# Kernel tuning notes

Measured on AMD Instinct MI355X. Metric: run time of the kernel, lower is better.

Reference implementation:

```python
import jax, jax.numpy as jnp
import numpy as np

EPS = 1e-5  # torch InstanceNorm2d default eps


def _attend(x_q, x_kv, Wq, Wk, Wv, Wo):
    # x_q, x_kv: [B, N, C]
    B, N, _ = x_q.shape
    q = x_q @ Wq            # [B, N, CH]
    k = x_kv @ Wk           # [B, N, CH]
    v = x_kv @ Wv           # [B, N, CH]
    CH = q.shape[-1]
    # rearrange 'b n c -> n (b c)' : [N, B*CH]; the torch repeat across batch
    # is redundant (same K/V for every query sample), so we keep one copy.
    kcat = jnp.transpose(k, (1, 0, 2)).reshape(N, B * CH)
    vcat = jnp.transpose(v, (1, 0, 2)).reshape(N, B * CH)
    # scores[b, i, j] = sum_n q[b, n, i] * kcat[n, j]  -> [B, CH, B*CH]
    scores = jnp.einsum('bni,nj->bij', q, kcat)
    # InstanceNorm2d(1): per-sample normalization over the (CH, B*CH) plane
    mu = scores.mean(axis=(1, 2), keepdims=True)
    var = scores.var(axis=(1, 2), keepdims=True)  # biased var, matches torch
    scores = (scores - mu) * jax.lax.rsqrt(var + EPS)
    attn = jax.nn.softmax(scores, axis=-1)        # softmax over j (dim=3)
    # ctx[b, n, i] = sum_j attn[b, i, j] * vcat[n, j]  -> [B, N, CH]
    ctx = jnp.einsum('bij,nj->bni', attn, vcat)
    return ctx @ Wo  # [B, N, C]


def setup_inputs() -> dict:
    key = jax.random.key(0)
    k0, k1, k2, k3, k4 = jax.random.split(key, 5)
    C, H = 64, 8
    CH = C * H
    emb = jax.random.normal(k0, (16, 2048, C), dtype=jnp.float32)
    s = 0.02
    Wq = jax.random.normal(k1, (C, CH), dtype=jnp.float32) * s
    Wk = jax.random.normal(k2, (C, CH), dtype=jnp.float32) * s
    Wv = jax.random.normal(k3, (C, CH), dtype=jnp.float32) * s
    Wo = jax.random.normal(k4, (CH, C), dtype=jnp.float32) * s
    return {"emb": emb, "Wq": Wq, "Wk": Wk, "Wv": Wv, "Wo": Wo}


def reference(emb, Wq, Wk, Wv, Wo):
    emb_l, emb_u = jnp.split(emb, 2, axis=0)
    emb_u_sg = jax.lax.stop_gradient(emb_u)  # emb_u is detached in the torch code
    out_u2l = _attend(emb_u_sg, emb_l, Wq, Wk, Wv, Wo)
    out_l2u = _attend(emb_l, emb_u_sg, Wq, Wk, Wv, Wo)
    return jnp.concatenate([out_l2u, out_u2l], axis=0)
```

## Files before the change

### kernel.cpp

```cpp
#include <hip/hip_runtime.h>
#include <hip/hip_fp16.h>

#define EPS 1e-5f

typedef __attribute__((ext_vector_type(8))) _Float16 half8;
typedef __attribute__((ext_vector_type(4))) _Float16 half4;
typedef __attribute__((ext_vector_type(4))) float float4v;

__device__ __forceinline__ float rv_from(const float* sums2, int db)
{
    float s1 = 0.f, s2 = 0.f;
#pragma unroll
    for (int p = 0; p < 8; p++) {
        s1 += sums2[(db * 8 + p) * 2];
        s2 += sums2[(db * 8 + p) * 2 + 1];
    }
    const float inv = 1.f / 2097152.f;
    float mu = s1 * inv;
    float var = s2 * inv - mu * mu;
    return rsqrtf(var + EPS);
}

__global__ __launch_bounds__(256)
void convT_k(const float* __restrict__ emb, const float* __restrict__ Wq,
             const float* __restrict__ Wk, const float* __restrict__ Wv,
             const float* __restrict__ Wo, __half* __restrict__ emb16,
             __half* __restrict__ embT16, __half* __restrict__ WkT16,
             __half* __restrict__ Wo16, __half* __restrict__ Wv16,
             float* __restrict__ GWQpart, float* __restrict__ wsp,
             __half* __restrict__ WqT16h, __half* __restrict__ WqT16l)
{
    __shared__ __align__(16) char smem[18432];
    const int tid = threadIdx.x;
    const int bid = blockIdx.x;

    if (bid < 256) {
        __half (*T)[136] = (__half(*)[136])smem;
        const int bb = bid >> 4;
        const int t0 = (bid & 15) * 128;
        const float* src = emb + (long long)bb * 131072 + (long long)t0 * 64;
        __half* d16 = emb16 + (long long)bb * 131072 + (long long)t0 * 64;
#pragma unroll
        for (int it = 0; it < 8; it++) {
            int e = (tid + it * 256) * 4;
            int t = e >> 6, c = e & 63;
            float4 v = *(const float4*)(src + t * 64 + c);
            half4 h;
            h[0] = (_Float16)v.x; h[1] = (_Float16)v.y;
            h[2] = (_Float16)v.z; h[3] = (_Float16)v.w;
            *(half4*)(d16 + t * 64 + c) = h;
            T[c + 0][t] = (__half)h[0];
            T[c + 1][t] = (__half)h[1];
            T[c + 2][t] = (__half)h[2];
            T[c + 3][t] = (__half)h[3];
        }
        __syncthreads();
        __half* dT = embT16 + (long long)bb * 131072 + t0;
#pragma unroll
        for (int it = 0; it < 4; it++) {
            int e = (tid + it * 256) * 8;
            int c = e >> 7, tt = e & 127;
            *(half8*)(dT + (long long)c * 2048 + tt) = *(const half8*)&T[c][tt];
        }
    } else if (bid < 272) {
        float (*t)[65] = (float(*)[65])smem;
        const int which = (bid - 256) >> 3;
        const int c0 = ((bid - 256) & 7) * 64;
        const int c = tid & 63, r4 = tid >> 6;
        if (which == 0) {
#pragma unroll
            for (int rr = r4; rr < 64; rr += 4)
                t[rr][c] = Wk[rr * 512 + c0 + c];
            __syncthreads();
#pragma unroll
            for (int rr = r4; rr < 64; rr += 4)
                WkT16[(c0 + rr) * 64 + c] = __float2half(t[c][rr]);
        } else {
#pragma unroll
            for (int rr = r4; rr < 64; rr += 4)
                t[rr][c] = Wo[(c0 + rr) * 64 + c];
            __syncthreads();
#pragma unroll
            for (int rr = r4; rr < 64; rr += 4)
                Wo16[rr * 512 + c0 + c] = __float2half(t[c][rr]);
        }
    } else if (bid < 280) {
        const int base = (bid - 272) * 4096;
#pragma unroll
        for (int it = 0; it < 4; it++) {
            int e = base + (tid + it * 256) * 4;
            float4 v = *(const float4*)(Wv + e);
            *(__half2*)(Wv16 + e)     = __floats2half2_rn(v.x, v.y);
            *(__half2*)(Wv16 + e + 2) = __floats2half2_rn(v.z, v.w);
        }
    } else if (bid < 296) {
        float (*Wl)[68] = (float(*)[68])smem;
        const int t2 = bid - 280;
        const int which = t2 >> 3;
        const int sl = t2 & 7;
        const int i0 = sl * 64;
        const float* W = which ? Wq : Wk;
        float* Gout = GWQpart + (long long)(which * 8 + sl) * 4096;
#pragma unroll
        for (int it = 0; it < 4; it++) {
            int e = tid + it * 256;
            int cc = e >> 4, i4 = (e & 15) * 4;
            *(float4*)&Wl[cc][i4] = *(const float4*)(W + cc * 512 + i0 + i4);
        }
        __syncthreads();
        if (tid < 64) {
            float s = 0.f;
#pragma unroll
            for (int j = 0; j < 64; j++) s += Wl[tid][j];
            wsp[(which * 8 + sl) * 64 + tid] = s;
        }
        const int cr = tid >> 2, cg = (tid & 3) * 16;
        float p[16] = {};
        for (int k = 0; k < 64; k++) {
            float a = Wl[cr][k];
#pragma unroll
            for (int j = 0; j < 16; j++) p[j] += a * Wl[cg + j][k];
        }
#pragma unroll
        for (int j = 0; j < 16; j++)
            Gout[cr * 64 + cg + j] = p[j];
    } else {
        float (*t)[65] = (float(*)[65])smem;
        const int i0 = (bid - 296) * 64;
        const int c = tid & 63, r4 = tid >> 6;
#pragma unroll
        for (int rr = r4; rr < 64; rr += 4)
            t[rr][c] = Wq[rr * 512 + i0 + c];
        __syncthreads();
#pragma unroll
        for (int rr = r4; rr < 64; rr += 4) {
            float x = t[c][rr];
            __half h = __float2half(x);
            WqT16h[(i0 + rr) * 64 + c] = h;
            WqT16l[(i0 + rr) * 64 + c] = __float2half(x - __half2float(h));
        }
    }
}

__global__ __launch_bounds__(256)
void gram_k(const __half* __restrict__ embT16, float* __restrict__ Gpart)
{
    const int tid = threadIdx.x, bid = blockIdx.x;
    const int ks = bid >> 6, z6 = bid & 63;
    const int b = z6 >> 3, bp = z6 & 7;
    const int lane = tid & 63, w = tid >> 6, q = lane >> 4, l16 = lane & 15;

    const __half* Arow = embT16 + (long long)b * 131072 +
                         (long long)(w * 16 + l16) * 2048 + ks * 256 + q * 8;
    const __half* Bbase = embT16 + 1048576 + (long long)bp * 131072 +
                          (long long)l16 * 2048 + ks * 256 + q * 8;

    float4v acc[4];
#pragma unroll
    for (int nt = 0; nt < 4; nt++) acc[nt] = (float4v)0.f;

#pragma unroll
    for (int t0 = 0; t0 < 256; t0 += 32) {
        half8 af = *(const half8*)(Arow + t0);
        half8 bf[4];
#pragma unroll
        for (int nt = 0; nt < 4; nt++)
            bf[nt] = *(const half8*)(Bbase + nt * 32768 + t0);
#pragma unroll
        for (int nt = 0; nt < 4; nt++)
            acc[nt] = __builtin_amdgcn_mfma_f32_16x16x32_f16(af, bf[nt], acc[nt], 0, 0, 0);
    }

    float* Gz = Gpart + (long long)ks * 262144 + (long long)z6 * 4096;
#pragma unroll
    for (int nt = 0; nt < 4; nt++)
#pragma unroll
        for (int t = 0; t < 4; t++) {
            int m = w * 16 + q * 4 + t;
            Gz[m * 64 + nt * 16 + l16] = acc[nt][t];
        }
}

__global__ __launch_bounds__(256)
void stats2_k(const float* __restrict__ Gpart, const float* __restrict__ GWQpart,
              const float* __restrict__ wsp, __half* __restrict__ GT16h,
              __half* __restrict__ GT16l, float* __restrict__ sums2)
{
    __shared__ float Graw[64][68], Gs[64][68], GQs[64][68], GWs[64][68];
    __shared__ float wqsS[64], wksS[64];
    const int tid = threadIdx.x;
    const int z = blockIdx.x;
    const int d = z >> 6, b = (z >> 3) & 7, bp = z & 7;
    const int zm = d ? (bp * 8 + b) : (b * 8 + bp);

    for (int f = tid * 4; f < 4096; f += 1024) {
        float4 g = make_float4(0.f, 0.f, 0.f, 0.f);
        float4 gw = g, gq = g;
#pragma unroll
        for (int s = 0; s < 8; s++) {
            float4 p = *(const float4*)(Gpart + (long long)s * 262144 + (long long)zm * 4096 + f);
            g.x += p.x; g.y += p.y; g.z += p.z; g.w += p.w;
            float4 w1 = *(const float4*)(GWQpart + (long long)s * 4096 + f);
            gw.x += w1.x; gw.y += w1.y; gw.z += w1.z; gw.w += w1.w;
            float4 q1 = *(const float4*)(GWQpart + (long long)(8 + s) * 4096 + f);
            gq.x += q1.x; gq.y += q1.y; gq.z += q1.z; gq.w += q1.w;
        }
        int rr = f >> 6, cc = f & 63;
        *(float4*)&Graw[rr][cc] = g;
        *(float4*)&GWs[rr][cc] = gw;
        *(float4*)&GQs[rr][cc] = gq;
    }
    if (tid < 64) {
        float a = 0.f, bsum = 0.f;
#pragma unroll
        for (int s = 0; s < 8; s++) {
            bsum += wsp[s * 64 + tid];
            a    += wsp[(8 + s) * 64 + tid];
        }
        wqsS[tid] = a; wksS[tid] = bsum;
    }
    __syncthreads();
    for (int e = tid; e < 4096; e += 256) {
        int rr = e >> 6, cc = e & 63;
        Gs[rr][cc] = d ? Graw[cc][rr] : Graw[rr][cc];
    }
    __syncthreads();
    for (int e = tid; e < 4096; e += 256) {
        int cp = e >> 6, c = e & 63;
        float g = Gs[c][cp];
        __half h = __float2half(g);
        GT16h[(long long)z * 4096 + e] = h;
        GT16l[(long long)z * 4096 + e] = __float2half(g - __half2float(h));
    }

    const int r = tid >> 2;
    const int c0 = (tid & 3) * 16;
    float p1[16] = {}, p2[16] = {};
    for (int k = 0; k < 64; k++) {
        float gq = GQs[r][k], g = Gs[r][k];
#pragma unroll
        for (int j = 0; j < 16; j++) {
            p1[j] += gq * Gs[k][c0 + j];
            p2[j] += g  * GWs[k][c0 + j];
        }
    }
    float s2 = 0.f;
#pragma unroll
    for (int j = 0; j < 16; j++) s2 += p1[j] * p2[j];
    float s1 = 0.f;
    const float wq = wqsS[r];
#pragma unroll
    for (int j = 0; j < 16; j++) s1 += wq * Gs[r][c0 + j] * wksS[c0 + j];

    const int lane = tid & 63, w = tid >> 6;
#pragma unroll
    for (int off = 32; off; off >>= 1) {
        s1 += __shfl_down(s1, off, 64);
        s2 += __shfl_down(s2, off, 64);
    }
    __shared__ float r1[4], r2[4];
    if (lane == 0) { r1[w] = s1; r2[w] = s2; }
    __syncthreads();
    if (tid == 0) {
        sums2[z * 2]     = r1[0] + r1[1] + r1[2] + r1[3];
        sums2[z * 2 + 1] = r2[0] + r2[1] + r2[2] + r2[3];
    }
}

__global__ __launch_bounds__(256)
void mfma_ms(const __half* __restrict__ WqT16h, const __half* __restrict__ WqT16l,
             const __half* __restrict__ GT16h, const __half* __restrict__ GT16l,
             const __half* __restrict__ WkT16, const __half* __restrict__ Wv16,
             const float* __restrict__ sums2, float* __restrict__ rsp,
             __half* __restrict__ Mt)
{
    __shared__ __half Es[128][72];
    __shared__ __half Wks[2][64][72];
    __shared__ __half Wvs[2][64][72];
    __shared__ __half Pt[128][72];

    const int tid = threadIdx.x;
    const int z = blockIdx.x;
    const int it = blockIdx.y;
    const int db = z >> 3, bp = z & 7;
    const int i0base = it * 128;

    const int lane = tid & 63, w = tid >> 6, q = lane >> 4, l16 = lane & 15;
    const float rv = rv_from(sums2, db);
    const int srow = tid >> 2, sc8 = (tid & 3) * 16;

    half8 gk0 = *(const half8*)(WkT16 + (long long)srow * 64 + sc8);
    half8 gk1 = *(const half8*)(WkT16 + (long long)srow * 64 + sc8 + 8);
    half8 gv0 = *(const half8*)(Wv16 + (long long)srow * 512 + sc8);
    half8 gv1 = *(const half8*)(Wv16 + (long long)srow * 512 + sc8 + 8);

    {
        const __half* Wh = WqT16h + (long long)i0base * 64;
        const __half* Wl = WqT16l + (long long)i0base * 64;
        const __half* Gh = GT16h + (long long)z * 4096;
        const __half* Gl = GT16l + (long long)z * 4096;
        float4v eacc[2][4];
#pragma unroll
        for (int a = 0; a < 2; a++)
#pragma unroll
            for (int b2 = 0; b2 < 4; b2++) eacc[a][b2] = (float4v)0.f;
#pragma unroll
        for (int kc = 0; kc < 64; kc += 32) {
            half8 ah[2], al[2], bh[4], bl[4];
#pragma unroll
            for (int mt = 0; mt < 2; mt++) {
                const int i = w * 32 + mt * 16 + l16;
                ah[mt] = *(const half8*)(Wh + i * 64 + kc + q * 8);
                al[mt] = *(const half8*)(Wl + i * 64 + kc + q * 8);
            }
#pragma unroll
            for (int nt = 0; nt < 4; nt++) {
                const int cp = nt * 16 + l16;
                bh[nt] = *(const half8*)(Gh + cp * 64 + kc + q * 8);
                bl[nt] = *(const half8*)(Gl + cp * 64 + kc + q * 8);
            }
#pragma unroll
            for (int mt = 0; mt < 2; mt++)
#pragma unroll
                for (int nt = 0; nt < 4; nt++) {
                    eacc[mt][nt] = __builtin_amdgcn_mfma_f32_16x16x32_f16(ah[mt], bh[nt], eacc[mt][nt], 0, 0, 0);
                    eacc[mt][nt] = __builtin_amdgcn_mfma_f32_16x16x32_f16(ah[mt], bl[nt], eacc[mt][nt], 0, 0, 0);
                    eacc[mt][nt] = __builtin_amdgcn_mfma_f32_16x16x32_f16(al[mt], bh[nt], eacc[mt][nt], 0, 0, 0);
                }
        }
#pragma unroll
        for (int mt = 0; mt < 2; mt++)
#pragma unroll
            for (int nt = 0; nt < 4; nt++)
#pragma unroll
                for (int t = 0; t < 4; t++)
                    Es[w * 32 + mt * 16 + q * 4 + t][nt * 16 + l16] =
                        __float2half(eacc[mt][nt][t]);
    }
    *(half8*)&Wks[0][srow][sc8]     = gk0;
    *(half8*)&Wks[0][srow][sc8 + 8] = gk1;
    *(half8*)&Wvs[0][srow][sc8]     = gv0;
    *(half8*)&Wvs[0][srow][sc8 + 8] = gv1;
    __syncthreads();

    float4v macc[2][4];
#pragma unroll
    for (int a = 0; a < 2; a++)
#pragma unroll
        for (int b2 = 0; b2 < 4; b2++) macc[a][b2] = (float4v)0.f;
    float rsacc[2] = {0.f, 0.f};

    int cur = 0;
    for (int c = 0; c < 8; c++) {
        const int ch0 = c * 64;
        if (c < 7) {
            const int chn = ch0 + 64;
            gk0 = *(const half8*)(WkT16 + (long long)(chn + srow) * 64 + sc8);
            gk1 = *(const half8*)(WkT16 + (long long)(chn + srow) * 64 + sc8 + 8);
            gv0 = *(const half8*)(Wv16 + (long long)srow * 512 + chn + sc8);
            gv1 = *(const half8*)(Wv16 + (long long)srow * 512 + chn + sc8 + 8);
        }

        float4v sacc[4][2];
#pragma unroll
        for (int a = 0; a < 4; a++)
#pragma unroll
            for (int b2 = 0; b2 < 2; b2++) sacc[a][b2] = (float4v)0.f;
#pragma unroll
        for (int kc = 0; kc < 64; kc += 32) {
            half8 af[4], bf[2];
#pragma unroll
            for (int mt = 0; mt < 4; mt++)
                af[mt] = *(const half8*)&Wks[cur][mt * 16 + l16][kc + q * 8];
#pragma unroll
            for (int nt = 0; nt < 2; nt++)
                bf[nt] = *(const half8*)&Es[w * 32 + nt * 16 + l16][kc + q * 8];
#pragma unroll
            for (int mt = 0; mt < 4; mt++)
#pragma unroll
                for (int nt = 0; nt < 2; nt++)
                    sacc[mt][nt] = __builtin_amdgcn_mfma_f32_16x16x32_f16(af[mt], bf[nt], sacc[mt][nt], 0, 0, 0);
        }

#pragma unroll
        for (int nt = 0; nt < 2; nt++) {
            const int i = w * 32 + nt * 16 + l16;
#pragma unroll
            for (int mt = 0; mt < 4; mt++) {
                float e0 = __expf(rv * sacc[mt][nt][0]);
                float e1 = __expf(rv * sacc[mt][nt][1]);
                float e2 = __expf(rv * sacc[mt][nt][2]);
                float e3 = __expf(rv * sacc[mt][nt][3]);
                rsacc[nt] += e0 + e1 + e2 + e3;
                const int ch = mt * 16 + q * 4;
                *(__half2*)&Pt[i][ch]     = __floats2half2_rn(e0, e1);
                *(__half2*)&Pt[i][ch + 2] = __floats2half2_rn(e2, e3);
            }
        }

#pragma unroll
        for (int kc = 0; kc < 64; kc += 32) {
            half8 af2[2], bf2[4];
#pragma unroll
            for (int mt2 = 0; mt2 < 2; mt2++)
                af2[mt2] = *(const half8*)&Pt[w * 32 + mt2 * 16 + l16][kc + q * 8];
#pragma unroll
            for (int nt2 = 0; nt2 < 4; nt2++)
                bf2[nt2] = *(const half8*)&Wvs[cur][nt2 * 16 + l16][kc + q * 8];
#pragma unroll
            for (int mt2 = 0; mt2 < 2; mt2++)
#pragma unroll
                for (int nt2 = 0; nt2 < 4; nt2++)
                    macc[mt2][nt2] = __builtin_amdgcn_mfma_f32_16x16x32_f16(af2[mt2], bf2[nt2], macc[mt2][nt2], 0, 0, 0);
        }

        if (c < 7) {
            *(half8*)&Wks[cur ^ 1][srow][sc8]     = gk0;
            *(half8*)&Wks[cur ^ 1][srow][sc8 + 8] = gk1;
            *(half8*)&Wvs[cur ^ 1][srow][sc8]     = gv0;
            *(half8*)&Wvs[cur ^ 1][srow][sc8 + 8] = gv1;
        }
        __syncthreads();
        cur ^= 1;
    }

#pragma unroll
    for (int nt = 0; nt < 2; nt++) {
        float p = rsacc[nt];
        p += __shfl_xor(p, 16, 64);
        p += __shfl_xor(p, 32, 64);
        if (q == 0)
            rsp[(long long)(db * 512 + i0base + w * 32 + nt * 16 + l16) * 8 + bp] = p;
    }

    __half (*MtS)[144] = (__half(*)[144])&Pt[0][0];
    const float sc = 1.f / 4096.f;
#pragma unroll
    for (int mt2 = 0; mt2 < 2; mt2++)
#pragma unroll
        for (int nt2 = 0; nt2 < 4; nt2++) {
            const int cp = nt2 * 16 + l16;
            const int il = w * 32 + mt2 * 16 + q * 4;
#pragma unroll
            for (int t = 0; t < 4; t++)
                MtS[cp][il + t] = __float2half(macc[mt2][nt2][t] * sc);
        }
    __syncthreads();
    __half* Mz = Mt + (long long)z * 32768;
    {
        const int row = tid >> 2, seg = (tid & 3) * 32;
#pragma unroll
        for (int j = 0; j < 4; j++)
            *(half8*)(Mz + (long long)row * 512 + i0base + seg + j * 8) =
                *(const half8*)&MtS[row][seg + j * 8];
    }
}

__global__ __launch_bounds__(256)
void mfma_n(const __half* __restrict__ Mt, const __half* __restrict__ Wo16,
            const float* __restrict__ rsp, __half* __restrict__ NT)
{
    __shared__ __half Mts[64][72];
    __shared__ __half Wos[64][72];
    __shared__ float invrS[64];
    const int tid = threadIdx.x;
    const int db = blockIdx.x >> 3, bp = blockIdx.x & 7;
    const __half* Mz = Mt + (long long)(db * 8 + bp) * 32768;
    const int lane = tid & 63, w = tid >> 6, q = lane >> 4, l16 = lane & 15;

    float4v acc[4];
#pragma unroll
    for (int mt = 0; mt < 4; mt++) acc[mt] = (float4v)0.f;

    const int srow = tid >> 2, sc8 = (tid & 3) * 16;

    for (int i0 = 0; i0 < 512; i0 += 64) {
        __syncthreads();
        if (tid < 64) {
            const float* rp = rsp + (long long)(db * 512 + i0 + tid) * 8;
            float4 a = *(const float4*)rp;
            float4 b = *(const float4*)(rp + 4);
            invrS[tid] = 4096.0f / (a.x + a.y + a.z + a.w + b.x + b.y + b.z + b.w);
        }
        __syncthreads();
#pragma unroll
        for (int h = 0; h < 2; h++) {
            half8 v = *(const half8*)(Mz + (long long)srow * 512 + i0 + sc8 + h * 8);
            half8 o;
#pragma unroll
            for (int j = 0; j < 8; j++)
                o[j] = (_Float16)((float)v[j] * invrS[sc8 + h * 8 + j]);
            *(half8*)&Mts[srow][sc8 + h * 8] = o;
            *(half8*)&Wos[srow][sc8 + h * 8] =
                *(const half8*)(Wo16 + (long long)srow * 512 + i0 + sc8 + h * 8);
        }
        __syncthreads();
#pragma unroll
        for (int kc = 0; kc < 64; kc += 32) {
            half8 af[4];
#pragma unroll
            for (int mt = 0; mt < 4; mt++)
                af[mt] = *(const half8*)&Mts[mt * 16 + l16][kc + q * 8];
            half8 bf = *(const half8*)&Wos[w * 16 + l16][kc + q * 8];
#pragma unroll
            for (int mt = 0; mt < 4; mt++)
                acc[mt] = __builtin_amdgcn_mfma_f32_16x16x32_f16(af[mt], bf, acc[mt], 0, 0, 0);
        }
    }

    __half* Nz = NT + (long long)db * 32768;
    const int o = w * 16 + l16;
#pragma unroll
    for (int mt = 0; mt < 4; mt++) {
        const int k = bp * 64 + mt * 16 + q * 4;
        *(__half2*)(Nz + (long long)o * 512 + k)     = __floats2half2_rn(acc[mt][0], acc[mt][1]);
        *(__half2*)(Nz + (long long)o * 512 + k + 2) = __floats2half2_rn(acc[mt][2], acc[mt][3]);
    }
}

__global__ __launch_bounds__(256)
void mfma_out(const __half* __restrict__ emb16, const __half* __restrict__ NT,
              float* __restrict__ out)
{
    const int tid = threadIdx.x;
    const int db = blockIdx.y;
    const int d = db >> 3;
    const int n0 = blockIdx.x * 128;
    const __half* Xb = emb16 + (long long)(1 - d) * 1048576;
    const __half* Bz = NT + (long long)db * 32768;

    const int lane = tid & 63, w = tid >> 6, q = lane >> 4, l16 = lane & 15;

    float4v acc[2][4];
#pragma unroll
    for (int a = 0; a < 2; a++)
#pragma unroll
        for (int b = 0; b < 4; b++) acc[a][b] = (float4v)0.f;

    for (int bp = 0; bp < 8; bp++) {
        const __half* src = Xb + (long long)bp * 131072 + (long long)n0 * 64;
#pragma unroll
        for (int kc = 0; kc < 64; kc += 32) {
            half8 af[2], bf[4];
#pragma unroll
            for (int mt = 0; mt < 2; mt++)
                af[mt] = *(const half8*)(src + (long long)(w * 32 + mt * 16 + l16) * 64 + kc + q * 8);
#pragma unroll
            for (int ot = 0; ot < 4; ot++)
                bf[ot] = *(const half8*)(Bz + (long long)(ot * 16 + l16) * 512 + bp * 64 + kc + q * 8);
#pragma unroll
            for (int mt = 0; mt < 2; mt++)
#pragma unroll
                for (int ot = 0; ot < 4; ot++)
                    acc[mt][ot] = __builtin_amdgcn_mfma_f32_16x16x32_f16(af[mt], bf[ot], acc[mt][ot], 0, 0, 0);
        }
    }

    float* Od = out + (long long)db * 131072;
#pragma unroll
    for (int mt = 0; mt < 2; mt++)
#pragma unroll
        for (int ot = 0; ot < 4; ot++)
#pragma unroll
            for (int t = 0; t < 4; t++) {
                int n = n0 + w * 32 + mt * 16 + q * 4 + t;
                Od[(long long)n * 64 + ot * 16 + l16] = acc[mt][ot][t];
            }
}

extern "C" void kernel_launch(void* const* d_in, const int* in_sizes, int n_in,
                              void* d_out, int out_size, void* d_ws, size_t ws_size,
                              hipStream_t stream)
{
    const float* emb = (const float*)d_in[0];
    const float* Wq  = (const float*)d_in[1];
    const float* Wk  = (const float*)d_in[2];
    const float* Wv  = (const float*)d_in[3];
    const float* Wo  = (const float*)d_in[4];
    float* out = (float*)d_out;
    float* ws  = (float*)d_ws;

    float* Gpart   = ws;
    float* GWQpart = ws + 2097152;
    float* wsp     = ws + 2162688;
    float* sums2   = ws + 2163712;
    __half* GT16h  = (__half*)(ws + 2163968);
    __half* GT16l  = (__half*)(ws + 2426112);
    float* rsp     = ws + 2688256;
    __half* WkT16  = (__half*)(ws + 2753792);
    __half* Wv16   = (__half*)(ws + 2770176);
    __half* Wo16   = (__half*)(ws + 2786560);
    __half* WqT16h = (__half*)(ws + 2802944);
    __half* WqT16l = (__half*)(ws + 2819328);
    __half* Mt     = (__half*)(ws + 2835712);
    __half* NT     = (__half*)(ws + 4932864);
    __half* emb16  = (__half*)(ws + 5195008);
    __half* embT16 = (__half*)(ws + 6243584);

    convT_k<<<304, 256, 0, stream>>>(emb, Wq, Wk, Wv, Wo, emb16, embT16,
                                     WkT16, Wo16, Wv16, GWQpart, wsp,
                                     WqT16h, WqT16l);

    gram_k<<<512, 256, 0, stream>>>(embT16, Gpart);

    stats2_k<<<128, 256, 0, stream>>>(Gpart, GWQpart, wsp, GT16h, GT16l, sums2);

    mfma_ms<<<dim3(128, 4), 256, 0, stream>>>(WqT16h, WqT16l, GT16h, GT16l,
                                              WkT16, Wv16, sums2, rsp, Mt);

    mfma_n<<<128, 256, 0, stream>>>(Mt, Wo16, rsp, NT);

    mfma_out<<<dim3(16, 16), 256, 0, stream>>>(emb16, NT, out);
}
```

Measured before the change: 156.9 us.

## Halve mfma_ms row tile to 64 and double grid for occupancy

```diff
diff --git a/kernel.cpp b/kernel.cpp
--- a/kernel.cpp
+++ b/kernel.cpp
@@ -267,23 +267,23 @@
     }
 }
 
-__global__ __launch_bounds__(256)
+__global__ __launch_bounds__(256, 4)
 void mfma_ms(const __half* __restrict__ WqT16h, const __half* __restrict__ WqT16l,
              const __half* __restrict__ GT16h, const __half* __restrict__ GT16l,
              const __half* __restrict__ WkT16, const __half* __restrict__ Wv16,
              const float* __restrict__ sums2, float* __restrict__ rsp,
              __half* __restrict__ Mt)
 {
-    __shared__ __half Es[128][72];
-    __shared__ __half Wks[2][64][72];
-    __shared__ __half Wvs[2][64][72];
-    __shared__ __half Pt[128][72];
+    __shared__ __half Es[64][72];
+    __shared__ __half Wks[64][72];
+    __shared__ __half Wvs[64][72];
+    __shared__ __half Pt[64][72];
 
     const int tid = threadIdx.x;
     const int z = blockIdx.x;
     const int it = blockIdx.y;
     const int db = z >> 3, bp = z & 7;
-    const int i0base = it * 128;
+    const int i0base = it * 64;
 
     const int lane = tid & 63, w = tid >> 6, q = lane >> 4, l16 = lane & 15;
     const float rv = rv_from(sums2, db);
@@ -299,19 +299,16 @@
         const __half* Wl = WqT16l + (long long)i0base * 64;
         const __half* Gh = GT16h + (long long)z * 4096;
         const __half* Gl = GT16l + (long long)z * 4096;
-        float4v eacc[2][4];
-#pragma unroll
-        for (int a = 0; a < 2; a++)
-#pragma unroll
-            for (int b2 = 0; b2 < 4; b2++) eacc[a][b2] = (float4v)0.f;
+        float4v eacc[4];
+#pragma unroll
+        for (int b2 = 0; b2 < 4; b2++) eacc[b2] = (float4v)0.f;
 #pragma unroll
         for (int kc = 0; kc < 64; kc += 32) {
-            half8 ah[2], al[2], bh[4], bl[4];
-#pragma unroll
-            for (int mt = 0; mt < 2; mt++) {
-                const int i = w * 32 + mt * 16 + l16;
-                ah[mt] = *(const half8*)(Wh + i * 64 + kc + q * 8);
-                al[mt] = *(const half8*)(Wl + i * 64 + kc + q * 8);
+            half8 ah, al, bh[4], bl[4];
+            {
+                const int i = w * 16 + l16;
+                ah = *(const half8*)(Wh + i * 64 + kc + q * 8);
+                al = *(const half8*)(Wl + i * 64 + kc + q * 8);
             }
 #pragma unroll
             for (int nt = 0; nt < 4; nt++) {
@@ -320,37 +317,29 @@
                 bl[nt] = *(const half8*)(Gl + cp * 64 + kc + q * 8);
             }
 #pragma unroll
-            for (int mt = 0; mt < 2; mt++)
-#pragma unroll
-                for (int nt = 0; nt < 4; nt++) {
-                    eacc[mt][nt] = __builtin_amdgcn_mfma_f32_16x16x32_f16(ah[mt], bh[nt], eacc[mt][nt], 0, 0, 0);
-                    eacc[mt][nt] = __builtin_amdgcn_mfma_f32_16x16x32_f16(ah[mt], bl[nt], eacc[mt][nt], 0, 0, 0);
-                    eacc[mt][nt] = __builtin_amdgcn_mfma_f32_16x16x32_f16(al[mt], bh[nt], eacc[mt][nt], 0, 0, 0);
-                }
-        }
-#pragma unroll
-        for (int mt = 0; mt < 2; mt++)
-#pragma unroll
-            for (int nt = 0; nt < 4; nt++)
-#pragma unroll
-                for (int t = 0; t < 4; t++)
-                    Es[w * 32 + mt * 16 + q * 4 + t][nt * 16 + l16] =
-                        __float2half(eacc[mt][nt][t]);
-    }
-    *(half8*)&Wks[0][srow][sc8]     = gk0;
-    *(half8*)&Wks[0][srow][sc8 + 8] = gk1;
-    *(half8*)&Wvs[0][srow][sc8]     = gv0;
-    *(half8*)&Wvs[0][srow][sc8 + 8] = gv1;
+            for (int nt = 0; nt < 4; nt++) {
+                eacc[nt] = __builtin_amdgcn_mfma_f32_16x16x32_f16(ah, bh[nt], eacc[nt], 0, 0, 0);
+                eacc[nt] = __builtin_amdgcn_mfma_f32_16x16x32_f16(ah, bl[nt], eacc[nt], 0, 0, 0);
+                eacc[nt] = __builtin_amdgcn_mfma_f32_16x16x32_f16(al, bh[nt], eacc[nt], 0, 0, 0);
+            }
+        }
+#pragma unroll
+        for (int nt = 0; nt < 4; nt++)
+#pragma unroll
+            for (int t = 0; t < 4; t++)
+                Es[w * 16 + q * 4 + t][nt * 16 + l16] = __float2half(eacc[nt][t]);
+    }
+    *(half8*)&Wks[srow][sc8]     = gk0;
+    *(half8*)&Wks[srow][sc8 + 8] = gk1;
+    *(half8*)&Wvs[srow][sc8]     = gv0;
+    *(half8*)&Wvs[srow][sc8 + 8] = gv1;
     __syncthreads();
 
-    float4v macc[2][4];
-#pragma unroll
-    for (int a = 0; a < 2; a++)
-#pragma unroll
-        for (int b2 = 0; b2 < 4; b2++) macc[a][b2] = (float4v)0.f;
-    float rsacc[2] = {0.f, 0.f};
-
-    int cur = 0;
+    float4v macc[4];
+#pragma unroll
+    for (int b2 = 0; b2 < 4; b2++) macc[b2] = (float4v)0.f;
+    float rsacc = 0.f;
+
     for (int c = 0; c < 8; c++) {
         const int ch0 = c * 64;
         if (c < 7) {
@@ -361,37 +350,30 @@
             gv1 = *(const half8*)(Wv16 + (long long)srow * 512 + chn + sc8 + 8);
         }
 
-        float4v sacc[4][2];
-#pragma unroll
-        for (int a = 0; a < 4; a++)
-#pragma unroll
-            for (int b2 = 0; b2 < 2; b2++) sacc[a][b2] = (float4v)0.f;
+        float4v sacc[4];
+#pragma unroll
+        for (int a = 0; a < 4; a++) sacc[a] = (float4v)0.f;
 #pragma unroll
         for (int kc = 0; kc < 64; kc += 32) {
-            half8 af[4], bf[2];
+            half8 af[4], bf;
 #pragma unroll
             for (int mt = 0; mt < 4; mt++)
-                af[mt] = *(const half8*)&Wks[cur][mt * 16 + l16][kc + q * 8];
-#pragma unroll
-            for (int nt = 0; nt < 2; nt++)
-                bf[nt] = *(const half8*)&Es[w * 32 + nt * 16 + l16][kc + q * 8];
+                af[mt] = *(const half8*)&Wks[mt * 16 + l16][kc + q * 8];
+            bf = *(const half8*)&Es[w * 16 + l16][kc + q * 8];
 #pragma unroll
             for (int mt = 0; mt < 4; mt++)
-#pragma unroll
-                for (int nt = 0; nt < 2; nt++)
-                    sacc[mt][nt] = __builtin_amdgcn_mfma_f32_16x16x32_f16(af[mt], bf[nt], sacc[mt][nt], 0, 0, 0);
-        }
-
-#pragma unroll
-        for (int nt = 0; nt < 2; nt++) {
-            const int i = w * 32 + nt * 16 + l16;
+                sacc[mt] = __builtin_amdgcn_mfma_f32_16x16x32_f16(af[mt], bf, sacc[mt], 0, 0, 0);
+        }
+
+        {
+            const int i = w * 16 + l16;
 #pragma unroll
             for (int mt = 0; mt < 4; mt++) {
-                float e0 = __expf(rv * sacc[mt][nt][0]);
-                float e1 = __expf(rv * sacc[mt][nt][1]);
-                float e2 = __expf(rv * sacc[mt][nt][2]);
-                float e3 = __expf(rv * sacc[mt][nt][3]);
-                rsacc[nt] += e0 + e1 + e2 + e3;
+                float e0 = __expf(rv * sacc[mt][0]);
+                float e1 = __expf(rv * sacc[mt][1]);
+                float e2 = __expf(rv * sacc[mt][2]);
+                float e3 = __expf(rv * sacc[mt][3]);
+                rsacc += e0 + e1 + e2 + e3;
                 const int ch = mt * 16 + q * 4;
                 *(__half2*)&Pt[i][ch]     = __floats2half2_rn(e0, e1);
                 *(__half2*)&Pt[i][ch + 2] = __floats2half2_rn(e2, e3);
@@ -400,57 +382,51 @@
 
 #pragma unroll
         for (int kc = 0; kc < 64; kc += 32) {
-            half8 af2[2], bf2[4];
-#pragma unroll
-            for (int mt2 = 0; mt2 < 2; mt2++)
-                af2[mt2] = *(const half8*)&Pt[w * 32 + mt2 * 16 + l16][kc + q * 8];
+            half8 af2, bf2[4];
+            af2 = *(const half8*)&Pt[w * 16 + l16][kc + q * 8];
 #pragma unroll
             for (int nt2 = 0; nt2 < 4; nt2++)
-                bf2[nt2] = *(const half8*)&Wvs[cur][nt2 * 16 + l16][kc + q * 8];
-#pragma unroll
-            for (int mt2 = 0; mt2 < 2; mt2++)
-#pragma unroll
-                for (int nt2 = 0; nt2 < 4; nt2++)
-                    macc[mt2][nt2] = __builtin_amdgcn_mfma_f32_16x16x32_f16(af2[mt2], bf2[nt2], macc[mt2][nt2], 0, 0, 0);
+                bf2[nt2] = *(const half8*)&Wvs[nt2 * 16 + l16][kc + q * 8];
+#pragma unroll
+            for (int nt2 = 0; nt2 < 4; nt2++)
+                macc[nt2] = __builtin_amdgcn_mfma_f32_16x16x32_f16(af2, bf2[nt2], macc[nt2], 0, 0, 0);
         }
 
         if (c < 7) {
-            *(half8*)&Wks[cur ^ 1][srow][sc8]     = gk0;
-            *(half8*)&Wks[cur ^ 1][srow][sc8 + 8] = gk1;
-            *(half8*)&Wvs[cur ^ 1][srow][sc8]     = gv0;
-            *(half8*)&Wvs[cur ^ 1][srow][sc8 + 8] = gv1;
-        }
-        __syncthreads();
-        cur ^= 1;
-    }
-
-#pragma unroll
-    for (int nt = 0; nt < 2; nt++) {
-        float p = rsacc[nt];
+            __syncthreads();
+            *(half8*)&Wks[srow][sc8]     = gk0;
+            *(half8*)&Wks[srow][sc8 + 8] = gk1;
+            *(half8*)&Wvs[srow][sc8]     = gv0;
+            *(half8*)&Wvs[srow][sc8 + 8] = gv1;
+            __syncthreads();
+        }
+    }
+
+    {
+        float p = rsacc;
         p += __shfl_xor(p, 16, 64);
         p += __shfl_xor(p, 32, 64);
         if (q == 0)
-            rsp[(long long)(db * 512 + i0base + w * 32 + nt * 16 + l16) * 8 + bp] = p;
-    }
-
-    __half (*MtS)[144] = (__half(*)[144])&Pt[0][0];
+            rsp[(long long)(db * 512 + i0base + w * 16 + l16) * 8 + bp] = p;
+    }
+    __syncthreads();
+
+    __half (*MtS)[72] = (__half(*)[72])&Pt[0][0];
     const float sc = 1.f / 4096.f;
 #pragma unroll
-    for (int mt2 = 0; mt2 < 2; mt2++)
-#pragma unroll
-        for (int nt2 = 0; nt2 < 4; nt2++) {
-            const int cp = nt2 * 16 + l16;
-            const int il = w * 32 + mt2 * 16 + q * 4;
-#pragma unroll
-            for (int t = 0; t < 4; t++)
-                MtS[cp][il + t] = __float2half(macc[mt2][nt2][t] * sc);
-        }
+    for (int nt2 = 0; nt2 < 4; nt2++) {
+        const int cp = nt2 * 16 + l16;
+        const int il = w * 16 + q * 4;
+#pragma unroll
+        for (int t = 0; t < 4; t++)
+            MtS[cp][il + t] = __float2half(macc[nt2][t] * sc);
+    }
     __syncthreads();
     __half* Mz = Mt + (long long)z * 32768;
     {
-        const int row = tid >> 2, seg = (tid & 3) * 32;
-#pragma unroll
-        for (int j = 0; j < 4; j++)
+        const int row = tid >> 2, seg = (tid & 3) * 16;
+#pragma unroll
+        for (int j = 0; j < 2; j++)
             *(half8*)(Mz + (long long)row * 512 + i0base + seg + j * 8) =
                 *(const half8*)&MtS[row][seg + j * 8];
     }
@@ -605,7 +581,7 @@
 
     stats2_k<<<128, 256, 0, stream>>>(Gpart, GWQpart, wsp, GT16h, GT16l, sums2);
 
-    mfma_ms<<<dim3(128, 4), 256, 0, stream>>>(WqT16h, WqT16l, GT16h, GT16l,
+    mfma_ms<<<dim3(128, 8), 256, 0, stream>>>(WqT16h, WqT16l, GT16h, GT16l,
                                               WkT16, Wv16, sums2, rsp, Mt);
 
     mfma_n<<<128, 256, 0, stream>>>(Mt, Wo16, rsp, NT);
```

Result: no change. 159.8 us (+1.8%).

## Fuse Gram split-K kernel into stats kernel, removing partial-sum buffer

Applied to the files above, without the earlier changes.

```diff
diff --git a/kernel.cpp b/kernel.cpp
--- a/kernel.cpp
+++ b/kernel.cpp
@@ -143,70 +143,57 @@
 }
 
 __global__ __launch_bounds__(256)
-void gram_k(const __half* __restrict__ embT16, float* __restrict__ Gpart)
-{
-    const int tid = threadIdx.x, bid = blockIdx.x;
-    const int ks = bid >> 6, z6 = bid & 63;
-    const int b = z6 >> 3, bp = z6 & 7;
-    const int lane = tid & 63, w = tid >> 6, q = lane >> 4, l16 = lane & 15;
-
-    const __half* Arow = embT16 + (long long)b * 131072 +
-                         (long long)(w * 16 + l16) * 2048 + ks * 256 + q * 8;
-    const __half* Bbase = embT16 + 1048576 + (long long)bp * 131072 +
-                          (long long)l16 * 2048 + ks * 256 + q * 8;
-
-    float4v acc[4];
-#pragma unroll
-    for (int nt = 0; nt < 4; nt++) acc[nt] = (float4v)0.f;
-
-#pragma unroll
-    for (int t0 = 0; t0 < 256; t0 += 32) {
-        half8 af = *(const half8*)(Arow + t0);
-        half8 bf[4];
-#pragma unroll
-        for (int nt = 0; nt < 4; nt++)
-            bf[nt] = *(const half8*)(Bbase + nt * 32768 + t0);
-#pragma unroll
-        for (int nt = 0; nt < 4; nt++)
-            acc[nt] = __builtin_amdgcn_mfma_f32_16x16x32_f16(af, bf[nt], acc[nt], 0, 0, 0);
-    }
-
-    float* Gz = Gpart + (long long)ks * 262144 + (long long)z6 * 4096;
-#pragma unroll
-    for (int nt = 0; nt < 4; nt++)
-#pragma unroll
-        for (int t = 0; t < 4; t++) {
-            int m = w * 16 + q * 4 + t;
-            Gz[m * 64 + nt * 16 + l16] = acc[nt][t];
-        }
-}
-
-__global__ __launch_bounds__(256)
-void stats2_k(const float* __restrict__ Gpart, const float* __restrict__ GWQpart,
-              const float* __restrict__ wsp, __half* __restrict__ GT16h,
-              __half* __restrict__ GT16l, float* __restrict__ sums2)
+void gramstats_k(const __half* __restrict__ embT16,
+                 const float* __restrict__ GWQpart, const float* __restrict__ wsp,
+                 __half* __restrict__ GT16h, __half* __restrict__ GT16l,
+                 float* __restrict__ sums2)
 {
     __shared__ float Graw[64][68], Gs[64][68], GQs[64][68], GWs[64][68];
     __shared__ float wqsS[64], wksS[64];
     const int tid = threadIdx.x;
     const int z = blockIdx.x;
     const int d = z >> 6, b = (z >> 3) & 7, bp = z & 7;
-    const int zm = d ? (bp * 8 + b) : (b * 8 + bp);
+    const int zb = d ? bp : b;
+    const int zp = d ? b : bp;
+
+    const int lane = tid & 63, w = tid >> 6, q = lane >> 4, l16 = lane & 15;
+
+    {
+        const __half* Arow = embT16 + (long long)zb * 131072 +
+                             (long long)(w * 16 + l16) * 2048 + q * 8;
+        const __half* Bbase = embT16 + 1048576 + (long long)zp * 131072 +
+                              (long long)l16 * 2048 + q * 8;
+        float4v acc[4];
+#pragma unroll
+        for (int nt = 0; nt < 4; nt++) acc[nt] = (float4v)0.f;
+        for (int t0 = 0; t0 < 2048; t0 += 32) {
+            half8 af = *(const half8*)(Arow + t0);
+            half8 bf[4];
+#pragma unroll
+            for (int nt = 0; nt < 4; nt++)
+                bf[nt] = *(const half8*)(Bbase + nt * 32768 + t0);
+#pragma unroll
+            for (int nt = 0; nt < 4; nt++)
+                acc[nt] = __builtin_amdgcn_mfma_f32_16x16x32_f16(af, bf[nt], acc[nt], 0, 0, 0);
+        }
+#pragma unroll
+        for (int nt = 0; nt < 4; nt++)
+#pragma unroll
+            for (int t = 0; t < 4; t++)
+                Graw[w * 16 + q * 4 + t][nt * 16 + l16] = acc[nt][t];
+    }
 
     for (int f = tid * 4; f < 4096; f += 1024) {
-        float4 g = make_float4(0.f, 0.f, 0.f, 0.f);
-        float4 gw = g, gq = g;
+        float4 gw = make_float4(0.f, 0.f, 0.f, 0.f);
+        float4 gq = gw;
 #pragma unroll
         for (int s = 0; s < 8; s++) {
-            float4 p = *(const float4*)(Gpart + (long long)s * 262144 + (long long)zm * 4096 + f);
-            g.x += p.x; g.y += p.y; g.z += p.z; g.w += p.w;
             float4 w1 = *(const float4*)(GWQpart + (long long)s * 4096 + f);
             gw.x += w1.x; gw.y += w1.y; gw.z += w1.z; gw.w += w1.w;
             float4 q1 = *(const float4*)(GWQpart + (long long)(8 + s) * 4096 + f);
             gq.x += q1.x; gq.y += q1.y; gq.z += q1.z; gq.w += q1.w;
         }
         int rr = f >> 6, cc = f & 63;
-        *(float4*)&Graw[rr][cc] = g;
         *(float4*)&GWs[rr][cc] = gw;
         *(float4*)&GQs[rr][cc] = gq;
     }
@@ -252,7 +239,6 @@
 #pragma unroll
     for (int j = 0; j < 16; j++) s1 += wq * Gs[r][c0 + j] * wksS[c0 + j];
 
-    const int lane = tid & 63, w = tid >> 6;
 #pragma unroll
     for (int off = 32; off; off >>= 1) {
         s1 += __shfl_down(s1, off, 64);
@@ -580,7 +566,6 @@
     float* out = (float*)d_out;
     float* ws  = (float*)d_ws;
 
-    float* Gpart   = ws;
     float* GWQpart = ws + 2097152;
     float* wsp     = ws + 2162688;
     float* sums2   = ws + 2163712;
@@ -601,9 +586,8 @@
                                      WkT16, Wo16, Wv16, GWQpart, wsp,
                                      WqT16h, WqT16l);
 
-    gram_k<<<512, 256, 0, stream>>>(embT16, Gpart);
-
-    stats2_k<<<128, 256, 0, stream>>>(Gpart, GWQpart, wsp, GT16h, GT16l, sums2);
+    gramstats_k<<<128, 256, 0, stream>>>(embT16, GWQpart, wsp,
+                                         GT16h, GT16l, sums2);
 
     mfma_ms<<<dim3(128, 4), 256, 0, stream>>>(WqT16h, WqT16l, GT16h, GT16l,
                                               WkT16, Wv16, sums2, rsp, Mt);
```

Measured after the change: 179.5 us. 1.14x slower.
